# Optimization experiments

Measured on AMD Instinct MI355X. Metric: run time of the kernel, lower is better.

## Reference

```python
import jax, jax.numpy as jnp
import numpy as np

Q_LEN = 2048
K_LEN = 2048
BATCH = 2
EMBED = 1024
HEADS = 16
HEAD_DIM = EMBED // HEADS
PE_ROWS = 2 * K_LEN


def _shift(p):
    # Transformer-XL pad/flatten shift: p is [B, H, Q, S] with S = 2*K-1 -> [B, H, Q, K]
    B, H, Q, S = p.shape
    pp = jnp.pad(p, ((0, 0), (0, 0), (0, 1), (0, 1)))          # [B,H,Q+1,S+1]
    flat = pp.reshape(B, H, (Q + 1) * (S + 1))
    flat = jax.lax.slice_in_dim(flat, S // 2, S // 2 + Q * S, axis=-1)
    return flat.reshape(B, H, Q, S)[..., : (S + 1) // 2]


def setup_inputs() -> dict:
    key = jax.random.key(0)
    ks = jax.random.split(key, 11)
    ws = 0.02  # weight scale
    inp = {
        "query": jax.random.normal(ks[0], (Q_LEN, BATCH, EMBED), jnp.float32),
        "key": jax.random.normal(ks[1], (K_LEN, BATCH, EMBED), jnp.float32),
        "value": jax.random.normal(ks[2], (K_LEN, BATCH, EMBED), jnp.float32),
        "pe": jax.random.normal(ks[3], (PE_ROWS, EMBED), jnp.float32),
        "w_q": jax.random.normal(ks[4], (EMBED, EMBED), jnp.float32) * ws,
        "w_k": jax.random.normal(ks[5], (EMBED, EMBED), jnp.float32) * ws,
        "w_v": jax.random.normal(ks[6], (EMBED, EMBED), jnp.float32) * ws,
        "w_k_pos": jax.random.normal(ks[7], (EMBED, EMBED), jnp.float32) * ws,
        "out_proj": jax.random.normal(ks[8], (EMBED, EMBED), jnp.float32) * ws,
        "content_bias": jax.random.normal(ks[9], (HEADS, HEAD_DIM), jnp.float32) * ws,
        "pos_bias": jax.random.normal(ks[10], (HEADS, HEAD_DIM), jnp.float32) * ws,
        "attn_mask": jnp.triu(jnp.ones((Q_LEN, K_LEN), dtype=bool), k=1),  # causal
    }
    return inp


def reference(query, key, value, pe, w_q, w_k, w_v, w_k_pos, out_proj,
              content_bias, pos_bias, attn_mask):
    Qlen, B, E = query.shape
    Klen = key.shape[0]
    H, D = content_bias.shape
    scaling = D ** -0.5

    # projections (torch Linear: x @ W^T); layout -> [B, H, L, D]
    q = (query @ w_q.T).reshape(Qlen, B, H, D).transpose(1, 2, 0, 3)
    k = (key @ w_k.T).reshape(Klen, B, H, D).transpose(1, 2, 0, 3)
    v = (value @ w_v.T).reshape(Klen, B, H, D).transpose(1, 2, 0, 3)

    # relative position keys: pe slice of size 2K-1 starting at pe.size(0)//2 - K + 1
    lower = pe.shape[0] // 2 - Klen + 1
    pe_slice = jax.lax.dynamic_slice_in_dim(pe, lower, 2 * Klen - 1, axis=0)
    k_pos = (pe_slice @ w_k_pos.T).reshape(2 * Klen - 1, H, D).transpose(1, 0, 2)  # [H, 2K-1, D]

    content = jnp.einsum('bhqd,bhkd->bhqk', q + content_bias[None, :, None, :], k)
    pos = jnp.einsum('bhqd,hsd->bhqs', q + pos_bias[None, :, None, :], k_pos)
    pos = _shift(pos)  # [B, H, Q, K]

    attn = (content + pos) * scaling
    attn = jnp.where(attn_mask[None, None], -jnp.inf, attn)
    w = jax.nn.softmax(attn, axis=-1)

    out = jnp.einsum('bhqk,bhkd->bhqd', w, v)
    out = out.transpose(2, 0, 1, 3).reshape(Qlen, B, E)
    return out @ out_proj.T
```

## Files before the change

kernel.cpp:

```cpp
#include <hip/hip_runtime.h>
#include <hip/hip_bf16.h>

typedef __hip_bfloat16 bf16;
typedef __attribute__((ext_vector_type(8))) short short8;
typedef __attribute__((ext_vector_type(8))) unsigned short u16x8;
typedef __attribute__((ext_vector_type(4))) float f32x4;

#define QL   2048
#define KLEN 2048
#define BATCH 2
#define EMB  1024
#define NH   16
#define HD   64
#define SPE  4095

__device__ __forceinline__ int detect_f32_wave(const void* __restrict__ p) {
    const ushort4 v = ((const ushort4*)p)[threadIdx.x & 63];
    int c = 0;
    c += __popcll(__ballot(((v.x >> 7) & 0xFF) >= 0x8A));
    c += __popcll(__ballot(((v.y >> 7) & 0xFF) >= 0x8A));
    c += __popcll(__ballot(((v.z >> 7) & 0xFF) >= 0x8A));
    c += __popcll(__ballot(((v.w >> 7) & 0xFF) >= 0x8A));
    return c >= 8;
}

__device__ __forceinline__ ushort4 cvt4(const void* src, long u4i, int f32) {
    ushort4 o;
    if (f32) {
        float4 v = ((const float4*)src)[u4i];
        bf16 a = (bf16)v.x, b = (bf16)v.y, c = (bf16)v.z, e = (bf16)v.w;
        o.x = *(unsigned short*)&a; o.y = *(unsigned short*)&b;
        o.z = *(unsigned short*)&c; o.w = *(unsigned short*)&e;
    } else {
        o = ((const ushort4*)src)[u4i];
    }
    return o;
}

__global__ __launch_bounds__(256) void conv_w(
    const void* w0, const void* w1, const void* w2, const void* w3, const void* w4,
    const void* cb, const void* pb, bf16* __restrict__ wdst)
{
    const int t = threadIdx.x;
    const int bid = blockIdx.x;
    __shared__ int f32s;
    if (bid < 1280) {
        const int seg = bid >> 8, inner = bid & 255;
        const void* src = seg == 0 ? w0 : seg == 1 ? w1 : seg == 2 ? w2 : seg == 3 ? w3 : w4;
        bf16* d = wdst + (size_t)seg * 1048576;
        if (t < 64) { int r = detect_f32_wave(src); if (t == 0) f32s = r; }
        __syncthreads();
        const int f32 = f32s;
#pragma unroll
        for (int i = 0; i < 4; i++) {
            long u4i = (long)inner * 1024 + i * 256 + t;
            ((ushort4*)d)[u4i] = cvt4(src, u4i, f32);
        }
    } else {
        if (t < 64) { int r = detect_f32_wave(cb); if (t == 0) f32s = r; }
        __syncthreads();
        const int f32 = f32s;
        ((ushort4*)(wdst + 5242880))[t]        = cvt4(cb, t, f32);
        ((ushort4*)(wdst + 5242880 + 1024))[t] = cvt4(pb, t, f32);
    }
}

__device__ __forceinline__ void llds16(const bf16* g, bf16* l) {
    __builtin_amdgcn_global_load_lds(
        (const __attribute__((address_space(1))) void*)g,
        (__attribute__((address_space(3))) void*)l,
        16, 0, 0);
}

__device__ __forceinline__ short8 pack_f32x8(const float4& a, const float4& b) {
    short8 o; bf16 x;
    x = (bf16)a.x; o[0] = *(short*)&x;  x = (bf16)a.y; o[1] = *(short*)&x;
    x = (bf16)a.z; o[2] = *(short*)&x;  x = (bf16)a.w; o[3] = *(short*)&x;
    x = (bf16)b.x; o[4] = *(short*)&x;  x = (bf16)b.y; o[5] = *(short*)&x;
    x = (bf16)b.z; o[6] = *(short*)&x;  x = (bf16)b.w; o[7] = *(short*)&x;
    return o;
}

template<bool F32>
struct AStage {
    u16x8  u[2];
    float4 f[2][2];
    __device__ __forceinline__ void load(const void* Av, const int go[2], int k0) {
#pragma unroll
        for (int i = 0; i < 2; i++) {
            int e = go[i] + k0;
            if (F32) {
                const float4* F = (const float4*)Av;
                f[i][0] = F[e >> 2];
                f[i][1] = F[(e >> 2) + 1];
            } else {
                u[i] = ((const u16x8*)Av)[e >> 3];
            }
        }
    }
    __device__ __forceinline__ void write(bf16* dst, int t) {
#pragma unroll
        for (int i = 0; i < 2; i++) {
            int c = i * 256 + t;
            short8 v;
            if (F32) v = pack_f32x8(f[i][0], f[i][1]);
            else     v = *(short8*)&u[i];
            *(short8*)&dst[c * 8] = v;
        }
    }
};

__device__ __forceinline__ void gcompute(
    const bf16* As, const bf16* Ws, int wr, int wc, int lm, int quad,
    f32x4 acc[4][8])
{
    short8 af[4], wf[8];
#pragma unroll
    for (int x = 0; x < 4; x++) {
        int ra = wr + x * 16 + lm;
        af[x] = *(const short8*)&As[ra * 32 + ((quad ^ (ra & 3)) * 8)];
    }
#pragma unroll
    for (int y = 0; y < 8; y++) {
        int rb = wc + y * 16 + lm;
        wf[y] = *(const short8*)&Ws[rb * 32 + ((quad ^ (rb & 3)) * 8)];
    }
#pragma unroll
    for (int mt = 0; mt < 4; mt++)
#pragma unroll
        for (int nt = 0; nt < 8; nt++)
            acc[mt][nt] = __builtin_amdgcn_mfma_f32_16x16x32_bf16(
                af[mt], wf[nt], acc[mt][nt], 0, 0, 0);
}

template<bool F32>
__device__ void gloop(
    const void* Av, const bf16* W, int m0, int n0, int mode,
    bf16* AsdB, bf16* WsdB,
    int t, int wr, int wc, int lm, int quad, f32x4 acc[4][8])
{
    int go[2];
#pragma unroll
    for (int i = 0; i < 2; i++) {
        int c = i * 256 + t, r = c >> 2, gc = (c & 3) ^ (r & 3);
        int ar = m0 + r;
        if (mode == 3) { ar = ar + 1; if (ar > 4095) ar = 4095; }
        go[i] = ar * 1024 + gc * 8;
    }
    auto stageW = [&](bf16* dst, int k0) {
#pragma unroll
        for (int i = 0; i < 4; i++) {
            int c = i * 256 + t, r = c >> 2, gc = (c & 3) ^ (r & 3);
            llds16(W + (size_t)(n0 + r) * 1024 + k0 + gc * 8, dst + (c & ~63) * 8);
        }
    };

    AStage<F32> s0, s1;
    s0.load(Av, go, 0);   stageW(WsdB,            0);
    s1.load(Av, go, 32);  stageW(WsdB + 256 * 32, 32);

#pragma unroll 1
    for (int it = 0; it < 32; ++it) {
        const int cur = it % 3;
        bf16* Ac = AsdB + cur * (128 * 32);
        bf16* Wc = WsdB + cur * (256 * 32);

        if (it == 31)       asm volatile("s_waitcnt vmcnt(0)" ::: "memory");
        else if constexpr (F32) asm volatile("s_waitcnt vmcnt(8)" ::: "memory");
        else                asm volatile("s_waitcnt vmcnt(6)" ::: "memory");

        if (it & 1) s1.write(Ac, t); else s0.write(Ac, t);

        asm volatile("s_waitcnt lgkmcnt(0)" ::: "memory");
        __builtin_amdgcn_s_barrier();
        __builtin_amdgcn_sched_barrier(0);

        if (it + 2 < 32) {
            const int nb = (it + 2) % 3;
            if (it & 1) s1.load(Av, go, (it + 2) * 32);
            else        s0.load(Av, go, (it + 2) * 32);
            stageW(WsdB + nb * (256 * 32), (it + 2) * 32);
        }
        gcompute(Ac, Wc, wr, wc, lm, quad, acc);
    }
}

__global__ __launch_bounds__(256, 2) void gemm_big(
    const void* __restrict__ Aq, const void* __restrict__ Ak,
    const void* __restrict__ Avv, const void* __restrict__ Ape,
    const bf16* __restrict__ ao, const bf16* __restrict__ wslab,
    bf16* __restrict__ qc, bf16* __restrict__ qp,
    bf16* __restrict__ kw, bf16* __restrict__ vw,
    bf16* __restrict__ kpos, float* __restrict__ outf, int mode_base)
{
    const int o = blockIdx.x;
    const int mode = mode_base + (o >> 7);
    const int s = (o >> 3) & 15;
    const int bx = (o & 7) + 8 * (s & 3);
    const int by = s >> 2;

    const void* A = mode == 0 ? Aq : mode == 1 ? Ak : mode == 2 ? Avv :
                    mode == 3 ? Ape : (const void*)ao;
    const bf16* W = wslab + (size_t)mode * 1048576;

    __shared__ __align__(16) bf16 Asd[3][128 * 32];
    __shared__ __align__(16) bf16 Wsd[3][256 * 32];
    __shared__ int f32s;

    const int t = threadIdx.x;
    const int w = t >> 6, lane = t & 63, lm = lane & 15, quad = lane >> 4;
    const int m0 = bx * 128, n0 = by * 256;
    const int wr = (w >> 1) * 64, wc = (w & 1) * 128;

    if (t < 64) { int r = detect_f32_wave(A); if (t == 0) f32s = r; }
    __syncthreads();

    f32x4 acc[4][8] = {};

    if (f32s) gloop<true >(A, W, m0, n0, mode, &Asd[0][0], &Wsd[0][0],
                           t, wr, wc, lm, quad, acc);
    else      gloop<false>(A, W, m0, n0, mode, &Asd[0][0], &Wsd[0][0],
                           t, wr, wc, lm, quad, acc);

    const bf16* cbb = wslab + 5242880;
    const bf16* pbb = wslab + 5242880 + 1024;

#pragma unroll
    for (int mt = 0; mt < 4; mt++) {
#pragma unroll
        for (int nt = 0; nt < 8; nt++) {
#pragma unroll
            for (int r4 = 0; r4 < 4; r4++) {
                int row = m0 + wr + mt * 16 + quad * 4 + r4;
                int col = n0 + wc + nt * 16 + lm;
                float v = acc[mt][nt][r4];
                if (mode == 0) {
                    int l = row >> 1, b = row & 1;
                    int h = col >> 6, d = col & 63;
                    size_t idx = ((size_t)(b * NH + h) * QL + l) * HD + d;
                    qc[idx] = (bf16)(v + __bfloat162float(cbb[col]));
                    qp[idx] = (bf16)(v + __bfloat162float(pbb[col]));
                } else if (mode == 1) {
                    int l = row >> 1, b = row & 1;
                    int h = col >> 6, d = col & 63;
                    kw[((size_t)(b * NH + h) * KLEN + l) * HD + d] = (bf16)v;
                } else if (mode == 2) {
                    int l = row >> 1, b = row & 1;
                    int h = col >> 6, d = col & 63;
                    vw[((size_t)(b * NH + h) * KLEN + l) * HD + d] = (bf16)v;
                } else if (mode == 3) {
                    if (row < SPE) {
                        int h = col >> 6, d = col & 63;
                        kpos[((size_t)h * SPE + row) * HD + d] = (bf16)v;
                    }
                } else {
                    outf[(size_t)row * 1024 + col] = v;
                }
            }
        }
    }
}

#define NEG_INF (-1.0e30f)
#define SCL2 0.18033688011f

__global__ __launch_bounds__(256) void attn_mfma(
    const bf16* __restrict__ qc_g, const bf16* __restrict__ qp_g,
    const bf16* __restrict__ k_g,  const bf16* __restrict__ v_g,
    const bf16* __restrict__ kpos_g, bf16* __restrict__ ao)
{
    const int lin = blockIdx.x + (blockIdx.y << 6) + (blockIdx.z << 10);
    const int xcd = lin & 7, s = lin >> 3;
    const int g   = (xcd << 2) | (s >> 6);
    const int u   = s & 63;
    const int bx  = 63 - u;
    const int h   = g & 15;
    const int b   = g >> 4;
    const int q0  = bx * 32;

    const bf16* qc_bh  = qc_g + ((size_t)(b * NH + h) * QL) * HD;
    const bf16* qp_bh  = qp_g + ((size_t)(b * NH + h) * QL) * HD;
    const bf16* k_bh   = k_g  + ((size_t)(b * NH + h) * KLEN) * HD;
    const bf16* v_bh   = v_g  + ((size_t)(b * NH + h) * KLEN) * HD;
    const bf16* kpos_h = kpos_g + (size_t)h * SPE * HD;

    __shared__ __align__(16) bf16 K_s [64 * 64];
    __shared__ __align__(16) bf16 Kp_s[96 * 64];
    __shared__ __align__(16) bf16 Vt_s[64 * 64];
    __shared__ __align__(16) bf16 Pb_s[32 * 64];
    __shared__ float Sc_s[32][69];
    __shared__ float Pt_s[32][98];
    __shared__ float arow_s[32];

    const int t = threadIdx.x;
    const int w = t >> 6, lane = t & 63, lm = lane & 15, quad = lane >> 4;

    const int sr = t >> 3;
    const int sc = (t & 7) * 8;
    const int vrr = t >> 3, vch = t & 7;
    const int vkc = vrr >> 2;

    const int mtc = w & 1;
    const int ntc = (w >> 1) * 2;
    const int mtp = w >> 1;
    const int ntp = (w & 1) * 3;

    float m_run = NEG_INF, l_part = 0.0f;
    f32x4 accO[2] = {{0,0,0,0},{0,0,0,0}};
    u16x8 vv0, vv1;

    const int nkt = (bx >> 1) + 1;

    short8 aQc0, aQc1, aQp0, aQp1;
    {
        const bf16* qr = qc_bh + (size_t)(q0 + mtc * 16 + lm) * HD;
        aQc0 = *(const short8*)(qr + quad * 8);
        aQc1 = *(const short8*)(qr + (4 + quad) * 8);
        const bf16* pr = qp_bh + (size_t)(q0 + mtp * 16 + lm) * HD;
        aQp0 = *(const short8*)(pr + quad * 8);
        aQp1 = *(const short8*)(pr + (4 + quad) * 8);
    }

#pragma unroll
    for (int i = 0; i < 2; i++) {
        int c = i * 256 + t, r = c >> 3, ch = c & 7, gc = ch ^ (r & 7);
        llds16(k_bh + (size_t)r * HD + gc * 8, K_s + (c & ~63) * 8);
    }
    {
        const int s0 = 2016 - q0;
#pragma unroll
        for (int i = 0; i < 3; i++) {
            int c = i * 256 + t, r = c >> 3, ch = c & 7, gc = ch ^ (r & 7);
            llds16(kpos_h + (size_t)(s0 + r) * HD + gc * 8, Kp_s + (c & ~63) * 8);
        }
    }
    vv0 = *(const u16x8*)&v_bh[(size_t)(2 * vrr)     * HD + vch * 8];
    vv1 = *(const u16x8*)&v_bh[(size_t)(2 * vrr + 1) * HD + vch * 8];

    for (int kt = 0; kt < nkt; kt++) {
        const int k0 = kt * 64;

        __syncthreads();

        {
            const int off = (2 * vrr) & 7;
#pragma unroll
            for (int j = 0; j < 8; j++) {
                unsigned int pair = (unsigned int)vv0[j] | ((unsigned int)vv1[j] << 16);
                int slot = vkc ^ vch ^ j;
                *(unsigned int*)&Vt_s[(vch * 8 + j) * 64 + slot * 8 + off] = pair;
            }
        }

        {
#pragma unroll
            for (int n = 0; n < 2; n++) {
                int rowB = (ntc + n) * 16 + lm;
                short8 b0 = *(const short8*)&K_s[rowB * 64 + ((quad)     ^ (rowB & 7)) * 8];
                short8 b1 = *(const short8*)&K_s[rowB * 64 + ((4 + quad) ^ (rowB & 7)) * 8];
                f32x4 acc = {0, 0, 0, 0};
                acc = __builtin_amdgcn_mfma_f32_16x16x32_bf16(aQc0, b0, acc, 0, 0, 0);
                acc = __builtin_amdgcn_mfma_f32_16x16x32_bf16(aQc1, b1, acc, 0, 0, 0);
#pragma unroll
                for (int r = 0; r < 4; r++)
                    Sc_s[mtc * 16 + quad * 4 + r][(ntc + n) * 16 + lm] = acc[r];
            }
        }
        {
#pragma unroll
            for (int n = 0; n < 3; n++) {
                int rowB = (ntp + n) * 16 + lm;
                short8 b0 = *(const short8*)&Kp_s[rowB * 64 + ((quad)     ^ (rowB & 7)) * 8];
                short8 b1 = *(const short8*)&Kp_s[rowB * 64 + ((4 + quad) ^ (rowB & 7)) * 8];
                f32x4 acc = {0, 0, 0, 0};
                acc = __builtin_amdgcn_mfma_f32_16x16x32_bf16(aQp0, b0, acc, 0, 0, 0);
                acc = __builtin_amdgcn_mfma_f32_16x16x32_bf16(aQp1, b1, acc, 0, 0, 0);
#pragma unroll
                for (int r = 0; r < 4; r++)
                    Pt_s[mtp * 16 + quad * 4 + r][(ntp + n) * 16 + lm] = acc[r];
            }
        }

        __syncthreads();

        if (kt + 1 < nkt) {
            const int k0n = k0 + 64;
            const int s0n = k0n - q0 + 2016;
#pragma unroll
            for (int i = 0; i < 2; i++) {
                int c = i * 256 + t, r = c >> 3, ch = c & 7, gc = ch ^ (r & 7);
                llds16(k_bh + (size_t)(k0n + r) * HD + gc * 8, K_s + (c & ~63) * 8);
            }
#pragma unroll
            for (int i = 0; i < 3; i++) {
                int c = i * 256 + t, r = c >> 3, ch = c & 7, gc = ch ^ (r & 7);
                llds16(kpos_h + (size_t)(s0n + r) * HD + gc * 8, Kp_s + (c & ~63) * 8);
            }
            vv0 = *(const u16x8*)&v_bh[(size_t)(k0n + 2 * vrr)     * HD + vch * 8];
            vv1 = *(const u16x8*)&v_bh[(size_t)(k0n + 2 * vrr + 1) * HD + vch * 8];
        }

        {
            float p[8];
            float pmax = NEG_INF;
#pragma unroll
            for (int j = 0; j < 8; j++) {
                int col = sc + j;
                float sv = (Sc_s[sr][col] + Pt_s[sr][col - sr + 31]) * SCL2;
                if (k0 + col > q0 + sr) sv = NEG_INF;
                p[j] = sv;
                pmax = fmaxf(pmax, sv);
            }
            float alpha = 1.0f;
            if (!__all(pmax <= m_run + 11.5f)) {
                float mx = pmax;
                mx = fmaxf(mx, __shfl_xor(mx, 1, 8));
                mx = fmaxf(mx, __shfl_xor(mx, 2, 8));
                mx = fmaxf(mx, __shfl_xor(mx, 4, 8));
                float mnew = fmaxf(m_run, mx);
                alpha = __builtin_amdgcn_exp2f(m_run - mnew);
                m_run = mnew;
            }
            float ls = 0.0f;
#pragma unroll
            for (int j = 0; j < 8; j++) {
                p[j] = __builtin_amdgcn_exp2f(p[j] - m_run);
                ls += p[j];
            }
            l_part = l_part * alpha + ls;
            if ((t & 7) == 0) arow_s[sr] = alpha;
            short8 pv;
#pragma unroll
            for (int j = 0; j < 8; j++) { bf16 x = (bf16)p[j]; pv[j] = *(short*)&x; }
            *(short8*)&Pb_s[sr * 64 + ((t & 7) ^ (sr & 7)) * 8] = pv;
        }

        asm volatile("s_waitcnt lgkmcnt(0)" ::: "memory");
        __builtin_amdgcn_s_barrier();
        __builtin_amdgcn_sched_barrier(0);

        {
            float al[4];
#pragma unroll
            for (int r = 0; r < 4; r++) al[r] = arow_s[mtc * 16 + quad * 4 + r];
            int rowA = mtc * 16 + lm;
            short8 a0 = *(const short8*)&Pb_s[rowA * 64 + ((quad)     ^ (rowA & 7)) * 8];
            short8 a1 = *(const short8*)&Pb_s[rowA * 64 + ((4 + quad) ^ (rowA & 7)) * 8];
#pragma unroll
            for (int n = 0; n < 2; n++) {
                int d = (ntc + n) * 16 + lm;
                int ds = (d >> 3) ^ (d & 7);
                short8 b0 = *(const short8*)&Vt_s[d * 64 + ((quad     ^ ds)) * 8];
                short8 b1 = *(const short8*)&Vt_s[d * 64 + (((4 + quad) ^ ds)) * 8];
#pragma unroll
                for (int r = 0; r < 4; r++) accO[n][r] *= al[r];
                accO[n] = __builtin_amdgcn_mfma_f32_16x16x32_bf16(a0, b0, accO[n], 0, 0, 0);
                accO[n] = __builtin_amdgcn_mfma_f32_16x16x32_bf16(a1, b1, accO[n], 0, 0, 0);
            }
        }
    }

    l_part += __shfl_xor(l_part, 1, 8);
    l_part += __shfl_xor(l_part, 2, 8);
    l_part += __shfl_xor(l_part, 4, 8);

    __syncthreads();
    if ((t & 7) == 0) arow_s[sr] = l_part;
    __syncthreads();

    float linv[4];
#pragma unroll
    for (int r = 0; r < 4; r++) linv[r] = 1.0f / arow_s[mtc * 16 + quad * 4 + r];
#pragma unroll
    for (int n = 0; n < 2; n++) {
#pragma unroll
        for (int r = 0; r < 4; r++) {
            int row = mtc * 16 + quad * 4 + r;
            ao[(((size_t)(q0 + row) * BATCH + b) * EMB) + h * HD + (ntc + n) * 16 + lm] =
                (bf16)(accO[n][r] * linv[r]);
        }
    }
}

extern "C" void kernel_launch(void* const* d_in, const int* in_sizes, int n_in,
                              void* d_out, int out_size, void* d_ws, size_t ws_size,
                              hipStream_t stream)
{
    const void* query = d_in[0];
    const void* key   = d_in[1];
    const void* value = d_in[2];
    const void* pe    = d_in[3];
    const void* w_q   = d_in[4];
    const void* w_k   = d_in[5];
    const void* w_v   = d_in[6];
    const void* w_kp  = d_in[7];
    const void* w_out = d_in[8];
    const void* cb    = d_in[9];
    const void* pb    = d_in[10];
    float* out = (float*)d_out;

    const size_t SLAB = 4194304;
    bf16* qc   = (bf16*)d_ws;
    bf16* qp   = qc + SLAB;
    bf16* kw   = qp + SLAB;
    bf16* vw   = kw + SLAB;
    bf16* kpos = vw + SLAB;
    bf16* ao   = kpos + SLAB;
    bf16* wqb  = ao + SLAB;

    dim3 blk(256);

    conv_w<<<dim3(1281), blk, 0, stream>>>(w_q, w_k, w_v, w_kp, w_out, cb, pb, wqb);

    gemm_big<<<dim3(512), blk, 0, stream>>>(
        query, key, value, pe, nullptr, wqb, qc, qp, kw, vw, kpos, nullptr, 0);

    attn_mfma<<<dim3(64, NH, BATCH), blk, 0, stream>>>(qc, qp, kw, vw, kpos, ao);

    gemm_big<<<dim3(128), blk, 0, stream>>>(
        query, key, value, pe, ao, wqb, qc, qp, kw, vw, kpos, out, 4);
}
```

Measured before the change: 384.2 us.

## Replace pipelined 128x256 GEMM with single-buffer 128x128x64 tiles and XCD-aware block remap

The projection GEMM drops its triple-buffered 128x256 tile with a K-step of 32 in favour of a single-buffered 128x128 tile with a K-step of 64. It waits on all loads before each compute phase. The grid becomes 3D with twice as many blocks, and block indices are permuted so that consecutive tiles spread across the 8 XCDs. The occupancy hint of 2 blocks per CU is also removed. The aim is more parallelism and smaller register and LDS footprint, but the change gives up load/compute overlap and lowers arithmetic intensity per block.

```diff
diff --git a/kernel.cpp b/kernel.cpp
--- a/kernel.cpp
+++ b/kernel.cpp
@@ -82,110 +82,74 @@
 }
 
 template<bool F32>
-struct AStage {
-    u16x8  u[2];
-    float4 f[2][2];
-    __device__ __forceinline__ void load(const void* Av, const int go[2], int k0) {
-#pragma unroll
-        for (int i = 0; i < 2; i++) {
-            int e = go[i] + k0;
+__device__ void gloop97(
+    const void* Av, const bf16* W, int m0, int n0, int mode,
+    bf16* Asd, bf16* Wsd,
+    int t, int wr, int wc, int lm, int quad, f32x4 acc[4][4])
+{
+    long go[4];
+#pragma unroll
+    for (int i = 0; i < 4; i++) {
+        int c = i * 256 + t, r = c >> 3, gc = (c & 7) ^ (r & 7);
+        int ar = m0 + r;
+        if (mode == 3) { ar = ar + 1; if (ar > 4095) ar = 4095; }
+        go[i] = (long)ar * 1024 + gc * 8;
+    }
+
+#pragma unroll 1
+    for (int k0 = 0; k0 < 1024; k0 += 64) {
+        u16x8 au[4]; float4 a32[4][2];
+#pragma unroll
+        for (int i = 0; i < 4; i++) {
+            long e = go[i] + k0;
             if (F32) {
                 const float4* F = (const float4*)Av;
-                f[i][0] = F[e >> 2];
-                f[i][1] = F[(e >> 2) + 1];
+                a32[i][0] = F[e >> 2];
+                a32[i][1] = F[(e >> 2) + 1];
             } else {
-                u[i] = ((const u16x8*)Av)[e >> 3];
-            }
-        }
-    }
-    __device__ __forceinline__ void write(bf16* dst, int t) {
-#pragma unroll
-        for (int i = 0; i < 2; i++) {
+                au[i] = ((const u16x8*)Av)[e >> 3];
+            }
+        }
+#pragma unroll
+        for (int i = 0; i < 4; i++) {
+            int c = i * 256 + t, r = c >> 3, gc = (c & 7) ^ (r & 7);
+            llds16(W + (size_t)(n0 + r) * 1024 + k0 + gc * 8, Wsd + (c & ~63) * 8);
+        }
+        asm volatile("s_waitcnt vmcnt(0)" ::: "memory");
+#pragma unroll
+        for (int i = 0; i < 4; i++) {
             int c = i * 256 + t;
             short8 v;
-            if (F32) v = pack_f32x8(f[i][0], f[i][1]);
-            else     v = *(short8*)&u[i];
-            *(short8*)&dst[c * 8] = v;
-        }
-    }
-};
-
-__device__ __forceinline__ void gcompute(
-    const bf16* As, const bf16* Ws, int wr, int wc, int lm, int quad,
-    f32x4 acc[4][8])
-{
-    short8 af[4], wf[8];
-#pragma unroll
-    for (int x = 0; x < 4; x++) {
-        int ra = wr + x * 16 + lm;
-        af[x] = *(const short8*)&As[ra * 32 + ((quad ^ (ra & 3)) * 8)];
-    }
-#pragma unroll
-    for (int y = 0; y < 8; y++) {
-        int rb = wc + y * 16 + lm;
-        wf[y] = *(const short8*)&Ws[rb * 32 + ((quad ^ (rb & 3)) * 8)];
-    }
-#pragma unroll
-    for (int mt = 0; mt < 4; mt++)
-#pragma unroll
-        for (int nt = 0; nt < 8; nt++)
-            acc[mt][nt] = __builtin_amdgcn_mfma_f32_16x16x32_bf16(
-                af[mt], wf[nt], acc[mt][nt], 0, 0, 0);
-}
-
-template<bool F32>
-__device__ void gloop(
-    const void* Av, const bf16* W, int m0, int n0, int mode,
-    bf16* AsdB, bf16* WsdB,
-    int t, int wr, int wc, int lm, int quad, f32x4 acc[4][8])
-{
-    int go[2];
-#pragma unroll
-    for (int i = 0; i < 2; i++) {
-        int c = i * 256 + t, r = c >> 2, gc = (c & 3) ^ (r & 3);
-        int ar = m0 + r;
-        if (mode == 3) { ar = ar + 1; if (ar > 4095) ar = 4095; }
-        go[i] = ar * 1024 + gc * 8;
-    }
-    auto stageW = [&](bf16* dst, int k0) {
-#pragma unroll
-        for (int i = 0; i < 4; i++) {
-            int c = i * 256 + t, r = c >> 2, gc = (c & 3) ^ (r & 3);
-            llds16(W + (size_t)(n0 + r) * 1024 + k0 + gc * 8, dst + (c & ~63) * 8);
-        }
-    };
-
-    AStage<F32> s0, s1;
-    s0.load(Av, go, 0);   stageW(WsdB,            0);
-    s1.load(Av, go, 32);  stageW(WsdB + 256 * 32, 32);
-
-#pragma unroll 1
-    for (int it = 0; it < 32; ++it) {
-        const int cur = it % 3;
-        bf16* Ac = AsdB + cur * (128 * 32);
-        bf16* Wc = WsdB + cur * (256 * 32);
-
-        if (it == 31)       asm volatile("s_waitcnt vmcnt(0)" ::: "memory");
-        else if constexpr (F32) asm volatile("s_waitcnt vmcnt(8)" ::: "memory");
-        else                asm volatile("s_waitcnt vmcnt(6)" ::: "memory");
-
-        if (it & 1) s1.write(Ac, t); else s0.write(Ac, t);
-
+            if (F32) v = pack_f32x8(a32[i][0], a32[i][1]);
+            else     v = *(short8*)&au[i];
+            *(short8*)&Asd[c * 8] = v;
+        }
         asm volatile("s_waitcnt lgkmcnt(0)" ::: "memory");
         __builtin_amdgcn_s_barrier();
         __builtin_amdgcn_sched_barrier(0);
 
-        if (it + 2 < 32) {
-            const int nb = (it + 2) % 3;
-            if (it & 1) s1.load(Av, go, (it + 2) * 32);
-            else        s0.load(Av, go, (it + 2) * 32);
-            stageW(WsdB + nb * (256 * 32), (it + 2) * 32);
-        }
-        gcompute(Ac, Wc, wr, wc, lm, quad, acc);
-    }
-}
-
-__global__ __launch_bounds__(256, 2) void gemm_big(
+#pragma unroll
+        for (int kk = 0; kk < 2; kk++) {
+            short8 af[4], wf[4];
+#pragma unroll
+            for (int x = 0; x < 4; x++) {
+                int ra = wr + x * 16 + lm;
+                af[x] = *(const short8*)&Asd[ra * 64 + (((kk * 4 + quad) ^ (ra & 7)) * 8)];
+                int rb = wc + x * 16 + lm;
+                wf[x] = *(const short8*)&Wsd[rb * 64 + (((kk * 4 + quad) ^ (rb & 7)) * 8)];
+            }
+#pragma unroll
+            for (int mt = 0; mt < 4; mt++)
+#pragma unroll
+                for (int nt = 0; nt < 4; nt++)
+                    acc[mt][nt] = __builtin_amdgcn_mfma_f32_16x16x32_bf16(
+                        af[mt], wf[nt], acc[mt][nt], 0, 0, 0);
+        }
+        __builtin_amdgcn_s_barrier();
+    }
+}
+
+__global__ __launch_bounds__(256) void gemm_big(
     const void* __restrict__ Aq, const void* __restrict__ Ak,
     const void* __restrict__ Avv, const void* __restrict__ Ape,
     const bf16* __restrict__ ao, const bf16* __restrict__ wslab,
@@ -193,34 +157,32 @@
     bf16* __restrict__ kw, bf16* __restrict__ vw,
     bf16* __restrict__ kpos, float* __restrict__ outf, int mode_base)
 {
-    const int o = blockIdx.x;
-    const int mode = mode_base + (o >> 7);
-    const int s = (o >> 3) & 15;
-    const int bx = (o & 7) + 8 * (s & 3);
-    const int by = s >> 2;
-
+    const int nwg = gridDim.x * gridDim.y * gridDim.z;
+    int lin = blockIdx.x + 32 * blockIdx.y + 256 * blockIdx.z;
+    lin = (lin & 7) * (nwg >> 3) + (lin >> 3);
+    const int bx = lin & 31, by = (lin >> 5) & 7, bz = lin >> 8;
+
+    const int mode = mode_base + bz;
     const void* A = mode == 0 ? Aq : mode == 1 ? Ak : mode == 2 ? Avv :
                     mode == 3 ? Ape : (const void*)ao;
     const bf16* W = wslab + (size_t)mode * 1048576;
 
-    __shared__ __align__(16) bf16 Asd[3][128 * 32];
-    __shared__ __align__(16) bf16 Wsd[3][256 * 32];
+    __shared__ __align__(16) bf16 Asd[128 * 64];
+    __shared__ __align__(16) bf16 Wsd[128 * 64];
     __shared__ int f32s;
 
     const int t = threadIdx.x;
     const int w = t >> 6, lane = t & 63, lm = lane & 15, quad = lane >> 4;
-    const int m0 = bx * 128, n0 = by * 256;
-    const int wr = (w >> 1) * 64, wc = (w & 1) * 128;
+    const int m0 = bx * 128, n0 = by * 128;
+    const int wr = (w >> 1) * 64, wc = (w & 1) * 64;
 
     if (t < 64) { int r = detect_f32_wave(A); if (t == 0) f32s = r; }
     __syncthreads();
 
-    f32x4 acc[4][8] = {};
-
-    if (f32s) gloop<true >(A, W, m0, n0, mode, &Asd[0][0], &Wsd[0][0],
-                           t, wr, wc, lm, quad, acc);
-    else      gloop<false>(A, W, m0, n0, mode, &Asd[0][0], &Wsd[0][0],
-                           t, wr, wc, lm, quad, acc);
+    f32x4 acc[4][4] = {};
+
+    if (f32s) gloop97<true >(A, W, m0, n0, mode, Asd, Wsd, t, wr, wc, lm, quad, acc);
+    else      gloop97<false>(A, W, m0, n0, mode, Asd, Wsd, t, wr, wc, lm, quad, acc);
 
     const bf16* cbb = wslab + 5242880;
     const bf16* pbb = wslab + 5242880 + 1024;
@@ -228,7 +190,7 @@
 #pragma unroll
     for (int mt = 0; mt < 4; mt++) {
 #pragma unroll
-        for (int nt = 0; nt < 8; nt++) {
+        for (int nt = 0; nt < 4; nt++) {
 #pragma unroll
             for (int r4 = 0; r4 < 4; r4++) {
                 int row = m0 + wr + mt * 16 + quad * 4 + r4;
@@ -512,11 +474,11 @@
 
     conv_w<<<dim3(1281), blk, 0, stream>>>(w_q, w_k, w_v, w_kp, w_out, cb, pb, wqb);
 
-    gemm_big<<<dim3(512), blk, 0, stream>>>(
+    gemm_big<<<dim3(32, 8, 4), blk, 0, stream>>>(
         query, key, value, pe, nullptr, wqb, qc, qp, kw, vw, kpos, nullptr, 0);
 
     attn_mfma<<<dim3(64, NH, BATCH), blk, 0, stream>>>(qc, qp, kw, vw, kpos, ao);
 
-    gemm_big<<<dim3(128), blk, 0, stream>>>(
+    gemm_big<<<dim3(32, 8, 1), blk, 0, stream>>>(
         query, key, value, pe, ao, wqb, qc, qp, kw, vw, kpos, out, 4);
 }
```

Result: faster. 359.2 us (-6.5%).
